# Kernel optimization log

Hardware: AMD Instinct MI355X
Metric: run time of the kernel (lower is better)

The kernel has to match this reference:

```python
import jax, jax.numpy as jnp
import numpy as np

VOCAB, TAGS, EMB, HID = 50257, 64, 512, 1024
B, S = 64, 512
H = HID // 2  # per-direction LSTM hidden size
NEG = -10000.0


def _lstm_dir(xs, w_ih, w_hh, b_ih, b_hh):
    # xs: (S, B, E) time-major. PyTorch gate order: i, f, g, o.
    pre = jnp.einsum('sbe,ge->sbg', xs, w_ih) + b_ih + b_hh  # (S, B, 4H)
    Bq = xs.shape[1]
    Hq = w_hh.shape[1]

    def step(carry, x_pre):
        h, c = carry
        g = x_pre + h @ w_hh.T
        i, f, gg, o = jnp.split(g, 4, axis=-1)
        c = jax.nn.sigmoid(f) * c + jax.nn.sigmoid(i) * jnp.tanh(gg)
        h = jax.nn.sigmoid(o) * jnp.tanh(c)
        return (h, c), h

    init = (jnp.zeros((Bq, Hq), xs.dtype), jnp.zeros((Bq, Hq), xs.dtype))
    _, hs = jax.lax.scan(step, init, pre)
    return hs  # (S, B, H)


def _crf_forward(emissions, transitions):
    # emissions: (B, S, T); returns log partition per batch element
    Bq, Sq, T = emissions.shape
    alpha0 = jnp.full((Bq, T), NEG, emissions.dtype).at[:, 0].set(0.0)

    def step(alpha, emit):
        # alpha: (B, T_prev); emit: (B, T_next)
        a = alpha[:, None, :] + transitions[None, :, :] + emit[:, :, None]
        return jax.scipy.special.logsumexp(a, axis=2), None

    alpha, _ = jax.lax.scan(step, alpha0, jnp.swapaxes(emissions, 0, 1))
    return jax.scipy.special.logsumexp(alpha, axis=1)


def _gold_score(emissions, tags, transitions):
    Bq = emissions.shape[0]
    tags_ext = jnp.concatenate(
        [jnp.zeros((Bq, 1), dtype=tags.dtype), tags], axis=1)  # (B, S+1)
    emit = jnp.take_along_axis(emissions, tags[:, :, None], axis=2)
    emit = emit[..., 0].sum(axis=1)  # (B,)
    trans = transitions[tags_ext[:, 1:], tags_ext[:, :-1]].sum(axis=1)  # (B,)
    return emit + trans


def setup_inputs() -> dict:
    key = jax.random.key(0)
    ks = jax.random.split(key, 16)
    sentences = jax.random.randint(ks[0], (B, S), 0, VOCAB)
    tags = jax.random.randint(ks[1], (B, S), 0, TAGS)
    lengths = jnp.full((B,), S, dtype=jnp.int32)

    sc = 1.0 / np.sqrt(H)
    u = lambda k, shp: jax.random.uniform(k, shp, jnp.float32, -sc, sc)
    emb = jax.random.normal(ks[2], (VOCAB, EMB), jnp.float32)
    emb = emb.at[0].set(0.0)  # padding_idx=0
    w_ih_f, w_hh_f = u(ks[3], (4 * H, EMB)), u(ks[4], (4 * H, H))
    b_ih_f, b_hh_f = u(ks[5], (4 * H,)), u(ks[6], (4 * H,))
    w_ih_b, w_hh_b = u(ks[7], (4 * H, EMB)), u(ks[8], (4 * H, H))
    b_ih_b, b_hh_b = u(ks[9], (4 * H,)), u(ks[10], (4 * H,))
    w_out = u(ks[11], (TAGS, HID))
    b_out = u(ks[12], (TAGS,))
    transitions = jax.random.normal(ks[13], (TAGS, TAGS), jnp.float32)
    transitions = transitions.at[:, 0].set(NEG).at[0, :].set(NEG)
    return dict(sentences=sentences, tags=tags, lengths=lengths, emb=emb,
                w_ih_f=w_ih_f, w_hh_f=w_hh_f, b_ih_f=b_ih_f, b_hh_f=b_hh_f,
                w_ih_b=w_ih_b, w_hh_b=w_hh_b, b_ih_b=b_ih_b, b_hh_b=b_hh_b,
                w_out=w_out, b_out=b_out, transitions=transitions)


def reference(sentences, tags, lengths, emb, w_ih_f, w_hh_f, b_ih_f, b_hh_f,
              w_ih_b, w_hh_b, b_ih_b, b_hh_b, w_out, b_out, transitions):
    x = emb[sentences]                       # (B, S, E)
    xs = jnp.swapaxes(x, 0, 1)               # (S, B, E) time-major
    h_f = _lstm_dir(xs, w_ih_f, w_hh_f, b_ih_f, b_hh_f)           # (S, B, H)
    h_b = _lstm_dir(xs[::-1], w_ih_b, w_hh_b, b_ih_b, b_hh_b)[::-1]
    lstm_out = jnp.concatenate([h_f, h_b], axis=-1)               # (S, B, 2H)
    lstm_out = jnp.swapaxes(lstm_out, 0, 1)                       # (B, S, 2H)
    emissions = lstm_out @ w_out.T + b_out                        # (B, S, T)
    gold = _gold_score(emissions, tags, transitions)
    fwd = _crf_forward(emissions, transitions)
    return jnp.mean(fwd - gold)
```

## Files before the change

kernel.cpp:

```cpp
#include <hip/hip_runtime.h>

#define NB 64
#define NS 512
#define NE 512
#define NH 512
#define NG 2048
#define NT 64
#define KC 1024
#define HB 16777216
#define SENT32 0x7FC07FC0u
#define NEGV (-10000.0f)

typedef __attribute__((ext_vector_type(8))) short bf16x8;
typedef __attribute__((ext_vector_type(4))) float f32x4;
typedef unsigned short u16;
typedef unsigned int u32;
typedef unsigned long long u64;

__device__ __forceinline__ u16 f2bf(float x) {
    unsigned u = __builtin_bit_cast(unsigned, x);
    u += 0x7fffu + ((u >> 16) & 1u);
    return (u16)(u >> 16);
}
__device__ __forceinline__ float sig_(float x) {
    return __builtin_amdgcn_rcpf(1.0f + __builtin_amdgcn_exp2f(-1.44269504f * x));
}
__device__ __forceinline__ float tanh_(float x) {
    return 2.0f * __builtin_amdgcn_rcpf(1.0f + __builtin_amdgcn_exp2f(-2.88539009f * x)) - 1.0f;
}

__global__ void prep_wcomb(const float* __restrict__ wihf, const float* __restrict__ whhf,
                           const float* __restrict__ wihb, const float* __restrict__ whhb,
                           u16* __restrict__ wcomb) {
    int idx = blockIdx.x * 256 + threadIdx.x;
    int base = idx * 4;
    int d = base >> 21;
    int rem = base & ((1 << 21) - 1);
    int n = rem >> 10;
    int k = rem & 1023;
    const float* wih = d ? wihb : wihf;
    const float* whh = d ? whhb : whhf;
    const float* src = (k < NE) ? (wih + n * NE + k) : (whh + n * NH + (k - NE));
    float4 v = *reinterpret_cast<const float4*>(src);
    ushort4 o;
    o.x = f2bf(v.x); o.y = f2bf(v.y); o.z = f2bf(v.z); o.w = f2bf(v.w);
    *reinterpret_cast<ushort4*>(wcomb + base) = o;
}

__global__ void prep_misc(const float* __restrict__ wout,
                          const float* __restrict__ bihf, const float* __restrict__ bhhf,
                          const float* __restrict__ bihb, const float* __restrict__ bhhb,
                          u16* __restrict__ woutbf, float* __restrict__ bias) {
    int idx = blockIdx.x * 256 + threadIdx.x;
    if (idx < 65536) { woutbf[idx] = f2bf(wout[idx]); return; }
    idx -= 65536;
    if (idx < 4096) {
        int d = idx >> 11, g = idx & 2047;
        bias[idx] = d ? (bihb[g] + bhhb[g]) : (bihf[g] + bhhf[g]);
    }
}

__global__ void prep_hfill(uint4* __restrict__ h) {
    int idx = blockIdx.x * 256 + threadIdx.x;
    uint4 v = {SENT32, SENT32, SENT32, SENT32};
    h[idx] = v;
}

__global__ void prep_embed(const float* __restrict__ emb, const int* __restrict__ sents,
                           u16* __restrict__ xbf) {
    int idx = blockIdx.x * 256 + threadIdx.x;
    int m = idx >> 7;
    int e = (idx & 127) << 2;
    int s = m >> 6, b = m & 63;
    int tok = sents[b * NS + s];
    float4 v = *reinterpret_cast<const float4*>(emb + (size_t)tok * NE + e);
    ushort4 o;
    o.x = f2bf(v.x); o.y = f2bf(v.y); o.z = f2bf(v.z); o.w = f2bf(v.w);
    *reinterpret_cast<ushort4*>(xbf + (size_t)m * NE + e) = o;
}

__global__ __launch_bounds__(512, 1)
void lstm_persist(const u16* __restrict__ xbf, const u16* __restrict__ wcomb,
                  const float* __restrict__ bias, u16* __restrict__ hall) {
    const int bh   = blockIdx.x >> 4;
    const int jblk = blockIdx.x & 15;
    const int dir  = blockIdx.y;
    const int t = threadIdx.x;
    const int w = t >> 6, l = t & 63;
    const int l16 = l & 15, lhi = l >> 4;
    const int kbase = w * 128;
    const bool isx = (w < 4);

    __shared__ float gred[8][32][134];

    bf16x8 bfrag[8][4];
#pragma unroll
    for (int nf = 0; nf < 8; ++nf)
#pragma unroll
        for (int kt = 0; kt < 4; ++kt) {
            int gr = (nf >> 1) * NH + jblk * 32 + (nf & 1) * 16 + l16;
            int k = kbase + kt * 32 + lhi * 8;
            bfrag[nf][kt] = *reinterpret_cast<const bf16x8*>(
                wcomb + (size_t)(dir * NG + gr) * KC + k);
        }

    const int row = t >> 4;
    const int jo  = t & 15;
    const int j0  = jo * 2;
    float breg[4][2];
#pragma unroll
    for (int gi = 0; gi < 4; ++gi)
#pragma unroll
        for (int u = 0; u < 2; ++u)
            breg[gi][u] = bias[dir * NG + gi * NH + jblk * 32 + j0 + u];
    float c0 = 0.f, c1 = 0.f;

    u32* Hw = reinterpret_cast<u32*>(hall) + (size_t)dir * (HB / 2);
    const u64* Hq = reinterpret_cast<const u64*>(hall) + (size_t)dir * (HB / 4);

    for (int step = 0; step < NS; ++step) {
        const int s = dir ? (NS - 1 - step) : step;
        const int sprev = dir ? (s + 1) : (s - 1);

        f32x4 acc[2][8];
#pragma unroll
        for (int mf = 0; mf < 2; ++mf)
#pragma unroll
            for (int nf = 0; nf < 8; ++nf)
                acc[mf][nf] = (f32x4){0.f, 0.f, 0.f, 0.f};

        if (isx) {
            const u16* Abase = xbf + (size_t)(s * NB + bh * 32) * NE + kbase;
#pragma unroll
            for (int kt = 0; kt < 4; ++kt) {
                int k = kt * 32 + lhi * 8;
#pragma unroll
                for (int mf = 0; mf < 2; ++mf) {
                    bf16x8 a = *reinterpret_cast<const bf16x8*>(Abase + (size_t)(mf * 16 + l16) * NE + k);
#pragma unroll
                    for (int nf = 0; nf < 8; ++nf)
                        acc[mf][nf] = __builtin_amdgcn_mfma_f32_16x16x32_bf16(a, bfrag[nf][kt], acc[mf][nf], 0, 0, 0);
                }
            }
        } else if (step > 0) {
            const int kloc = kbase - 512;
            u64 qa[4][2], qb[4][2];
            u32 okm = 0;
#pragma unroll
            for (int kt = 0; kt < 4; ++kt) {
                int j = kloc + kt * 32 + lhi * 8;
#pragma unroll
                for (int mf = 0; mf < 2; ++mf) {
                    const u64* P = Hq + (size_t)(sprev * NB + bh * 32 + mf * 16 + l16) * 128 + (j >> 2);
                    u64 v0 = __hip_atomic_load(P,     __ATOMIC_RELAXED, __HIP_MEMORY_SCOPE_AGENT);
                    u64 v1 = __hip_atomic_load(P + 1, __ATOMIC_RELAXED, __HIP_MEMORY_SCOPE_AGENT);
                    qa[kt][mf] = v0; qb[kt][mf] = v1;
                    bool bad = ((u32)v0 == SENT32) | ((u32)(v0 >> 32) == SENT32)
                             | ((u32)v1 == SENT32) | ((u32)(v1 >> 32) == SENT32);
                    okm |= (bad ? 0u : 1u) << (kt * 2 + mf);
                }
            }
            while (__ballot(okm != 0xFFu)) {
                __builtin_amdgcn_s_sleep(1);
#pragma unroll
                for (int kt = 0; kt < 4; ++kt) {
                    int j = kloc + kt * 32 + lhi * 8;
#pragma unroll
                    for (int mf = 0; mf < 2; ++mf) {
                        u32 bit = 1u << (kt * 2 + mf);
                        if (!(okm & bit)) {
                            const u64* P = Hq + (size_t)(sprev * NB + bh * 32 + mf * 16 + l16) * 128 + (j >> 2);
                            u64 v0 = __hip_atomic_load(P,     __ATOMIC_RELAXED, __HIP_MEMORY_SCOPE_AGENT);
                            u64 v1 = __hip_atomic_load(P + 1, __ATOMIC_RELAXED, __HIP_MEMORY_SCOPE_AGENT);
                            qa[kt][mf] = v0; qb[kt][mf] = v1;
                            bool bad = ((u32)v0 == SENT32) | ((u32)(v0 >> 32) == SENT32)
                                     | ((u32)v1 == SENT32) | ((u32)(v1 >> 32) == SENT32);
                            if (!bad) okm |= bit;
                        }
                    }
                }
            }
            __builtin_amdgcn_sched_barrier(0);
#pragma unroll
            for (int kt = 0; kt < 4; ++kt) {
#pragma unroll
                for (int mf = 0; mf < 2; ++mf) {
                    union { u64 q[2]; bf16x8 v; } cv;
                    cv.q[0] = qa[kt][mf]; cv.q[1] = qb[kt][mf];
#pragma unroll
                    for (int nf = 0; nf < 8; ++nf)
                        acc[mf][nf] = __builtin_amdgcn_mfma_f32_16x16x32_bf16(cv.v, bfrag[nf][kt], acc[mf][nf], 0, 0, 0);
                }
            }
        }

#pragma unroll
        for (int mf = 0; mf < 2; ++mf)
#pragma unroll
            for (int nf = 0; nf < 8; ++nf)
#pragma unroll
                for (int r = 0; r < 4; ++r)
                    gred[w][mf * 16 + lhi * 4 + r][nf * 16 + l16] = acc[mf][nf][r];
        __syncthreads();

        float g[2][4];
#pragma unroll
        for (int u = 0; u < 2; ++u)
#pragma unroll
            for (int gi = 0; gi < 4; ++gi) {
                int n = gi * 32 + j0 + u;
                float sum = gred[0][row][n];
#pragma unroll
                for (int kw = 1; kw < 8; ++kw) sum += gred[kw][row][n];
                g[u][gi] = sum + breg[gi][u];
            }
        float cn0 = sig_(g[0][1]) * c0 + sig_(g[0][0]) * tanh_(g[0][2]);
        float cn1 = sig_(g[1][1]) * c1 + sig_(g[1][0]) * tanh_(g[1][2]);
        c0 = cn0; c1 = cn1;
        u32 hw = (u32)f2bf(sig_(g[0][3]) * tanh_(cn0))
               | ((u32)f2bf(sig_(g[1][3]) * tanh_(cn1)) << 16);
        __hip_atomic_store(Hw + (size_t)(s * NB + bh * 32 + row) * 256 + jblk * 16 + jo, hw,
                           __ATOMIC_RELAXED, __HIP_MEMORY_SCOPE_AGENT);
        __syncthreads();
    }
}

__global__ void emis_kernel(const u16* __restrict__ hall, const u16* __restrict__ woutbf,
                            const float* __restrict__ bout, float* __restrict__ emis) {
    const int blk = blockIdx.x;
    const int t = threadIdx.x;
    const int w = t >> 6, l = t & 63;
    const int l16 = l & 15, lhi = l >> 4;

    const u16* arow0 = hall + (size_t)(blk * 64 + w * 16 + l16) * NH;
    const u16* arow1 = arow0 + HB;
    const u16* br0 = woutbf + (size_t)(0 * 16 + l16) * KC;
    const u16* br1 = woutbf + (size_t)(1 * 16 + l16) * KC;
    const u16* br2 = woutbf + (size_t)(2 * 16 + l16) * KC;
    const u16* br3 = woutbf + (size_t)(3 * 16 + l16) * KC;

    f32x4 a0 = {0.f,0.f,0.f,0.f}, a1 = {0.f,0.f,0.f,0.f}, a2 = {0.f,0.f,0.f,0.f}, a3 = {0.f,0.f,0.f,0.f};
#pragma unroll
    for (int kt = 0; kt < 16; ++kt) {
        int k = kt * 32 + lhi * 8;
        bf16x8 a = *reinterpret_cast<const bf16x8*>(arow0 + k);
        a0 = __builtin_amdgcn_mfma_f32_16x16x32_bf16(a, *reinterpret_cast<const bf16x8*>(br0 + k), a0, 0, 0, 0);
        a1 = __builtin_amdgcn_mfma_f32_16x16x32_bf16(a, *reinterpret_cast<const bf16x8*>(br1 + k), a1, 0, 0, 0);
        a2 = __builtin_amdgcn_mfma_f32_16x16x32_bf16(a, *reinterpret_cast<const bf16x8*>(br2 + k), a2, 0, 0, 0);
        a3 = __builtin_amdgcn_mfma_f32_16x16x32_bf16(a, *reinterpret_cast<const bf16x8*>(br3 + k), a3, 0, 0, 0);
    }
#pragma unroll
    for (int kt = 0; kt < 16; ++kt) {
        int k = kt * 32 + lhi * 8;
        bf16x8 a = *reinterpret_cast<const bf16x8*>(arow1 + k);
        a0 = __builtin_amdgcn_mfma_f32_16x16x32_bf16(a, *reinterpret_cast<const bf16x8*>(br0 + NH + k), a0, 0, 0, 0);
        a1 = __builtin_amdgcn_mfma_f32_16x16x32_bf16(a, *reinterpret_cast<const bf16x8*>(br1 + NH + k), a1, 0, 0, 0);
        a2 = __builtin_amdgcn_mfma_f32_16x16x32_bf16(a, *reinterpret_cast<const bf16x8*>(br2 + NH + k), a2, 0, 0, 0);
        a3 = __builtin_amdgcn_mfma_f32_16x16x32_bf16(a, *reinterpret_cast<const bf16x8*>(br3 + NH + k), a3, 0, 0, 0);
    }
#pragma unroll
    for (int r = 0; r < 4; ++r) {
        int gm = blk * 64 + w * 16 + lhi * 4 + r;
        emis[(size_t)gm * NT + 0 * 16 + l16] = a0[r] + bout[0 * 16 + l16];
        emis[(size_t)gm * NT + 1 * 16 + l16] = a1[r] + bout[1 * 16 + l16];
        emis[(size_t)gm * NT + 2 * 16 + l16] = a2[r] + bout[2 * 16 + l16];
        emis[(size_t)gm * NT + 3 * 16 + l16] = a3[r] + bout[3 * 16 + l16];
    }
}

__global__ void gold_kernel(const float* __restrict__ emis, const int* __restrict__ tags,
                            const float* __restrict__ trans, float* __restrict__ gold) {
    int b = blockIdx.x, t = threadIdx.x;
    float acc = 0.f;
    for (int s = t; s < NS; s += 256) {
        int tag = tags[b * NS + s];
        int prev = (s == 0) ? 0 : tags[b * NS + s - 1];
        acc += emis[(size_t)(s * NB + b) * NT + tag] + trans[tag * NT + prev];
    }
    acc += __shfl_xor(acc, 1);  acc += __shfl_xor(acc, 2);  acc += __shfl_xor(acc, 4);
    acc += __shfl_xor(acc, 8);  acc += __shfl_xor(acc, 16); acc += __shfl_xor(acc, 32);
    __shared__ float red[4];
    if ((t & 63) == 0) red[t >> 6] = acc;
    __syncthreads();
    if (t == 0) gold[b] = red[0] + red[1] + red[2] + red[3];
}

__global__ void crf_kernel(const float* __restrict__ emis, const float* __restrict__ trans,
                           float* __restrict__ fwd) {
    int b = blockIdx.x, l = threadIdx.x;
    float Tc[64];
#pragma unroll
    for (int p = 0; p < 64; ++p)
        Tc[p] = trans[l * NT + p];
    float a = (l == 0) ? 0.f : NEGV;

    for (int s = 0; s < NS; ++s) {
        float emit = emis[(size_t)(s * NB + b) * NT + l];
        float M = -3.0e38f;
#pragma unroll
        for (int p = 0; p < 64; ++p)
            M = fmaxf(M, __shfl(a, p) + Tc[p]);
        float S = 0.f;
#pragma unroll
        for (int p = 0; p < 64; ++p)
            S += __builtin_amdgcn_exp2f((__shfl(a, p) + Tc[p] - M) * 1.44269504f);
        a = M + __builtin_amdgcn_logf(S) * 0.69314718f + emit;
    }
    float M = a;
#pragma unroll
    for (int d = 1; d < 64; d <<= 1) M = fmaxf(M, __shfl_xor(M, d));
    float e = __builtin_amdgcn_exp2f((a - M) * 1.44269504f);
#pragma unroll
    for (int d = 1; d < 64; d <<= 1) e += __shfl_xor(e, d);
    if (l == 0) fwd[b] = M + __builtin_amdgcn_logf(e) * 0.69314718f;
}

__global__ void final_kernel(const float* __restrict__ fwd, const float* __restrict__ gold,
                             float* __restrict__ out) {
    int t = threadIdx.x;
    float v = fwd[t] - gold[t];
    for (int d = 1; d < 64; d <<= 1) v += __shfl_xor(v, d);
    if (t == 0) out[0] = v * (1.0f / 64.0f);
}

extern "C" void kernel_launch(void* const* d_in, const int* in_sizes, int n_in,
                              void* d_out, int out_size, void* d_ws, size_t ws_size,
                              hipStream_t stream) {
    (void)in_sizes; (void)n_in; (void)out_size; (void)ws_size;
    const int* sents = (const int*)d_in[0];
    const int* tags  = (const int*)d_in[1];
    const float* emb  = (const float*)d_in[3];
    const float* wihf = (const float*)d_in[4];
    const float* whhf = (const float*)d_in[5];
    const float* bihf = (const float*)d_in[6];
    const float* bhhf = (const float*)d_in[7];
    const float* wihb = (const float*)d_in[8];
    const float* whhb = (const float*)d_in[9];
    const float* bihb = (const float*)d_in[10];
    const float* bhhb = (const float*)d_in[11];
    const float* wout = (const float*)d_in[12];
    const float* bout = (const float*)d_in[13];
    const float* trans = (const float*)d_in[14];

    char* ws = (char*)d_ws;
    u16*   WCOMB  = (u16*)(ws + 0);
    u16*   WOUTBF = (u16*)(ws + 8388608);
    float* BIAS   = (float*)(ws + 8519680);
    u16*   XBF    = (u16*)(ws + 8536064);
    u16*   HALL   = (u16*)(ws + 42090496);
    float* EMIS   = (float*)(ws + 109199360);
    float* FWD    = (float*)(ws + 117587968);
    float* GOLD   = (float*)(ws + 117588224);

    prep_wcomb<<<4096, 256, 0, stream>>>(wihf, whhf, wihb, whhb, WCOMB);
    prep_misc<<<272, 256, 0, stream>>>(wout, bihf, bhhf, bihb, bhhb, WOUTBF, BIAS);
    prep_hfill<<<16384, 256, 0, stream>>>((uint4*)HALL);
    prep_embed<<<16384, 256, 0, stream>>>(emb, sents, XBF);

    lstm_persist<<<dim3(32, 2), 512, 0, stream>>>(XBF, WCOMB, BIAS, HALL);

    emis_kernel<<<512, 256, 0, stream>>>(HALL, WOUTBF, bout, EMIS);
    gold_kernel<<<64, 256, 0, stream>>>(EMIS, tags, trans, GOLD);
    crf_kernel<<<64, 64, 0, stream>>>(EMIS, trans, FWD);
    final_kernel<<<1, 64, 0, stream>>>(FWD, GOLD, (float*)d_out);
}
```

Baseline: 3.625 ms.

## Double LSTM block width to 1024 threads, bf16 partial sums, prefetch CRF emissions

The persistent LSTM kernel now runs 32 blocks of 1024 threads instead of 64 blocks of 512. Each block covers 64 hidden units using two wave groups of 8 k-split waves, which halves the number of blocks polling for each step's hidden state. The cross-wave gate reduction buffer is stored as bf16 instead of fp32 so the doubled tile still fits in LDS, at the cost of precision in the gate pre-activations. The CRF kernel also prefetches the next step's emission one iteration ahead to hide the load latency.

After: 13.32 ms. 268% more time.

```diff
diff --git a/kernel.cpp b/kernel.cpp
--- a/kernel.cpp
+++ b/kernel.cpp
@@ -21,6 +21,9 @@
     unsigned u = __builtin_bit_cast(unsigned, x);
     u += 0x7fffu + ((u >> 16) & 1u);
     return (u16)(u >> 16);
+}
+__device__ __forceinline__ float bf2f(u16 x) {
+    return __builtin_bit_cast(float, (u32)x << 16);
 }
 __device__ __forceinline__ float sig_(float x) {
     return __builtin_amdgcn_rcpf(1.0f + __builtin_amdgcn_exp2f(-1.44269504f * x));
@@ -79,40 +82,44 @@
     *reinterpret_cast<ushort4*>(xbf + (size_t)m * NE + e) = o;
 }
 
-__global__ __launch_bounds__(512, 1)
+__global__ __launch_bounds__(1024, 1)
 void lstm_persist(const u16* __restrict__ xbf, const u16* __restrict__ wcomb,
                   const float* __restrict__ bias, u16* __restrict__ hall) {
-    const int bh   = blockIdx.x >> 4;
-    const int jblk = blockIdx.x & 15;
+    const int bh   = blockIdx.x >> 3;
+    const int jblk = blockIdx.x & 7;
     const int dir  = blockIdx.y;
     const int t = threadIdx.x;
     const int w = t >> 6, l = t & 63;
     const int l16 = l & 15, lhi = l >> 4;
-    const int kbase = w * 128;
-    const bool isx = (w < 4);
-
-    __shared__ float gred[8][32][134];
+    const int kw = w & 7;
+    const int jh = w >> 3;
+    const bool isx = (kw < 4);
+
+    __shared__ u16 gred[2][8][32][136];
 
     bf16x8 bfrag[8][4];
 #pragma unroll
     for (int nf = 0; nf < 8; ++nf)
 #pragma unroll
         for (int kt = 0; kt < 4; ++kt) {
-            int gr = (nf >> 1) * NH + jblk * 32 + (nf & 1) * 16 + l16;
-            int k = kbase + kt * 32 + lhi * 8;
+            int gr = (nf >> 1) * NH + jblk * 64 + jh * 32 + (nf & 1) * 16 + l16;
+            int k = kw * 128 + kt * 32 + lhi * 8;
             bfrag[nf][kt] = *reinterpret_cast<const bf16x8*>(
                 wcomb + (size_t)(dir * NG + gr) * KC + k);
         }
 
-    const int row = t >> 4;
-    const int jo  = t & 15;
-    const int j0  = jo * 2;
+    const int row = t >> 5;
+    const int jc  = t & 31;
+    const int j0  = jc * 2;
+    const int jhE = j0 >> 5;
+    const int chE = (j0 & 31) >> 4;
+    const int clE = j0 & 15;
     float breg[4][2];
 #pragma unroll
     for (int gi = 0; gi < 4; ++gi)
 #pragma unroll
         for (int u = 0; u < 2; ++u)
-            breg[gi][u] = bias[dir * NG + gi * NH + jblk * 32 + j0 + u];
+            breg[gi][u] = bias[dir * NG + gi * NH + jblk * 64 + j0 + u];
     float c0 = 0.f, c1 = 0.f;
 
     u32* Hw = reinterpret_cast<u32*>(hall) + (size_t)dir * (HB / 2);
@@ -130,7 +137,7 @@
                 acc[mf][nf] = (f32x4){0.f, 0.f, 0.f, 0.f};
 
         if (isx) {
-            const u16* Abase = xbf + (size_t)(s * NB + bh * 32) * NE + kbase;
+            const u16* Abase = xbf + (size_t)(s * NB + bh * 32) * NE + kw * 128;
 #pragma unroll
             for (int kt = 0; kt < 4; ++kt) {
                 int k = kt * 32 + lhi * 8;
@@ -143,7 +150,7 @@
                 }
             }
         } else if (step > 0) {
-            const int kloc = kbase - 512;
+            const int kloc = (kw - 4) * 128;
             u64 qa[4][2], qb[4][2];
             u32 okm = 0;
 #pragma unroll
@@ -200,26 +207,29 @@
             for (int nf = 0; nf < 8; ++nf)
 #pragma unroll
                 for (int r = 0; r < 4; ++r)
-                    gred[w][mf * 16 + lhi * 4 + r][nf * 16 + l16] = acc[mf][nf][r];
+                    gred[jh][kw][mf * 16 + lhi * 4 + r][nf * 16 + l16] = f2bf(acc[mf][nf][r]);
         __syncthreads();
 
         float g[2][4];
 #pragma unroll
-        for (int u = 0; u < 2; ++u)
-#pragma unroll
-            for (int gi = 0; gi < 4; ++gi) {
-                int n = gi * 32 + j0 + u;
-                float sum = gred[0][row][n];
-#pragma unroll
-                for (int kw = 1; kw < 8; ++kw) sum += gred[kw][row][n];
-                g[u][gi] = sum + breg[gi][u];
-            }
+        for (int gi = 0; gi < 4; ++gi) {
+            int col = (gi * 2 + chE) * 16 + clE;
+            float s0 = 0.f, s1 = 0.f;
+#pragma unroll
+            for (int kw2 = 0; kw2 < 8; ++kw2) {
+                u32 pr = *reinterpret_cast<const u32*>(&gred[jhE][kw2][row][col]);
+                s0 += bf2f((u16)pr);
+                s1 += bf2f((u16)(pr >> 16));
+            }
+            g[0][gi] = s0 + breg[gi][0];
+            g[1][gi] = s1 + breg[gi][1];
+        }
         float cn0 = sig_(g[0][1]) * c0 + sig_(g[0][0]) * tanh_(g[0][2]);
         float cn1 = sig_(g[1][1]) * c1 + sig_(g[1][0]) * tanh_(g[1][2]);
         c0 = cn0; c1 = cn1;
         u32 hw = (u32)f2bf(sig_(g[0][3]) * tanh_(cn0))
                | ((u32)f2bf(sig_(g[1][3]) * tanh_(cn1)) << 16);
-        __hip_atomic_store(Hw + (size_t)(s * NB + bh * 32 + row) * 256 + jblk * 16 + jo, hw,
+        __hip_atomic_store(Hw + (size_t)(s * NB + bh * 32 + row) * 256 + jblk * 32 + jc, hw,
                            __ATOMIC_RELAXED, __HIP_MEMORY_SCOPE_AGENT);
         __syncthreads();
     }
@@ -294,8 +304,11 @@
         Tc[p] = trans[l * NT + p];
     float a = (l == 0) ? 0.f : NEGV;
 
+    float emit_next = emis[(size_t)(0 * NB + b) * NT + l];
     for (int s = 0; s < NS; ++s) {
-        float emit = emis[(size_t)(s * NB + b) * NT + l];
+        float emit = emit_next;
+        if (s + 1 < NS)
+            emit_next = emis[(size_t)((s + 1) * NB + b) * NT + l];
         float M = -3.0e38f;
 #pragma unroll
         for (int p = 0; p < 64; ++p)
@@ -357,7 +370,7 @@
     prep_hfill<<<16384, 256, 0, stream>>>((uint4*)HALL);
     prep_embed<<<16384, 256, 0, stream>>>(emb, sents, XBF);
 
-    lstm_persist<<<dim3(32, 2), 512, 0, stream>>>(XBF, WCOMB, BIAS, HALL);
+    lstm_persist<<<dim3(16, 2), 1024, 0, stream>>>(XBF, WCOMB, BIAS, HALL);
 
     emis_kernel<<<512, 256, 0, stream>>>(HALL, WOUTBF, bout, EMIS);
     gold_kernel<<<64, 256, 0, stream>>>(EMIS, tags, trans, GOLD);
```
